# Performance work log

Measured on AMD Instinct MI355X. Metric: run time of the kernel, lower is better.

Reference implementation:

```python
import jax, jax.numpy as jnp
import numpy as np

B, D_IN, HID, DEPTH = 16384, 128, 16, 8
N_INNER = 2 ** DEPTH - 1   # 255
N_LEAF = 2 ** DEPTH        # 256


def setup_inputs() -> dict:
    key = jax.random.key(0)
    ks = jax.random.split(key, 4)
    x = jax.random.normal(ks[0], (B, D_IN), jnp.float32)
    # Batched per-inner-node tiny MLP parameters (PyTorch stores one Sequential per node;
    # we stack them along a leading node axis so the math is identical but vectorized).
    W1 = jax.random.normal(ks[1], (N_INNER, D_IN, HID), jnp.float32) / np.sqrt(D_IN).astype(np.float32)
    b1 = jnp.zeros((N_INNER, HID), jnp.float32)
    W2 = jax.random.normal(ks[2], (N_INNER, HID), jnp.float32) / np.sqrt(HID).astype(np.float32)
    b2 = jnp.zeros((N_INNER,), jnp.float32)
    leaf = jax.random.normal(ks[3], (N_LEAF, 1), jnp.float32) * 0.1
    return {"x": x, "W1": W1, "b1": b1, "W2": W2, "b2": b2, "leaf": leaf}


def reference(x, W1, b1, W2, b2, leaf):
    b = x.shape[0]
    depth = int(np.log2(leaf.shape[0]))
    # All inner-node gates in one batched GEMM: p[b, n] = sigmoid(W2_n . relu(W1_n^T x_b + b1_n) + b2_n)
    h1 = jax.nn.relu(jnp.einsum('bi,nih->bnh', x, W1) + b1[None])  # [B, N_inner, hid]
    p = jax.nn.sigmoid(jnp.einsum('bnh,nh->bn', h1, W2) + b2[None])  # [B, N_inner]

    # Level-by-level probability propagation (heap-ordered nodes):
    # children of node j are 2j+1 (left, mass*(1-p)) and 2j+2 (right, mass*p).
    r = jnp.ones((b, 1), x.dtype)
    levels = []
    for l in range(depth):
        levels.append(r)
        pl = p[:, 2 ** l - 1: 2 ** (l + 1) - 1]  # probs of nodes at level l, [B, 2^l]
        # interleave (left, right) so child ordering matches heap indexing
        r = jnp.stack([r * (1.0 - pl), r * pl], axis=-1).reshape(b, 2 ** (l + 1))
    node_reach = jnp.concatenate(levels, axis=1)  # [B, N_inner]
    path_probs = r                                 # [B, N_leaf]

    h = (path_probs @ leaf)[:, 0]                  # [B]
    return (h, path_probs, p, node_reach)
```

## Files before the change

### kernel.cpp

```cpp
#include <hip/hip_runtime.h>

#define BATCH 16384
#define DIN   128
#define HIDN  16
#define NNODE 255
#define NLEAF 256

typedef _Float16 half8 __attribute__((ext_vector_type(8)));
typedef _Float16 half4 __attribute__((ext_vector_type(4)));
typedef float   float4v __attribute__((ext_vector_type(4)));

__global__ __launch_bounds__(256) void k_pack(const float* __restrict__ x, const float* __restrict__ w1,
                                              const float* __restrict__ w2,
                                              half8* __restrict__ xp, half8* __restrict__ w1p,
                                              _Float16* __restrict__ w2h) {
    __shared__ float w[DIN * 17];
    int t = threadIdx.x;
    if (blockIdx.x < 1024) {
        int gid  = blockIdx.x * 256 + t;
        int lane = gid & 63;
        int kc   = (gid >> 6) & 3;
        int bt   = gid >> 8;
        const float4* src = (const float4*)(x + (size_t)(bt * 16 + (lane & 15)) * DIN + kc * 32 + ((lane >> 4) * 8));
        float4 v0 = src[0], v1 = src[1];
        half8 v;
        v[0] = (_Float16)v0.x; v[1] = (_Float16)v0.y; v[2] = (_Float16)v0.z; v[3] = (_Float16)v0.w;
        v[4] = (_Float16)v1.x; v[5] = (_Float16)v1.y; v[6] = (_Float16)v1.z; v[7] = (_Float16)v1.w;
        xp[gid] = v;
    } else {
        int n = blockIdx.x - 1024;
        const float4* src = (const float4*)(w1 + (size_t)n * (DIN * HIDN)) + t * 2;
        float4 a0 = src[0], a1 = src[1];
        int base = t * 8;
#pragma unroll
        for (int e = 0; e < 4; ++e) {
            int idx0 = base + e, idx1 = base + 4 + e;
            w[(idx0 >> 4) * 17 + (idx0 & 15)] = (&a0.x)[e];
            w[(idx1 >> 4) * 17 + (idx1 & 15)] = (&a1.x)[e];
        }
        __syncthreads();
        int L  = t & 63;
        int kc = t >> 6;
        int m  = L & 15;
        int k0 = kc * 32 + (L >> 4) * 8;
        half8 v;
#pragma unroll
        for (int j = 0; j < 8; ++j) v[j] = (_Float16)w[(k0 + j) * 17 + m];
        w1p[(size_t)n * 256 + t] = v;
        if (t < HIDN) w2h[n * HIDN + t] = (_Float16)w2[n * HIDN + t];
    }
}

__global__ __launch_bounds__(512, 2) void k_fused(const half8* __restrict__ xp, const half8* __restrict__ w1p,
                                                  const float* __restrict__ b1, const _Float16* __restrict__ w2h,
                                                  const float* __restrict__ b2, const float* __restrict__ leaf,
                                                  float* __restrict__ h_out, float* __restrict__ pp_out,
                                                  float* __restrict__ p_out, float* __restrict__ nr_out) {
    __shared__ float sp[64][260];
    int wv   = threadIdx.x >> 6;
    int lane = threadIdx.x & 63;
    int q    = lane >> 4;
    int bt0  = blockIdx.x * 4;

    half8 bq[4][4];
#pragma unroll
    for (int t = 0; t < 4; ++t)
#pragma unroll
        for (int kc = 0; kc < 4; ++kc)
            bq[t][kc] = xp[(size_t)((bt0 + t) * 4 + kc) * 64 + lane];
    asm volatile("" ::: "memory");

    int cnt = (wv < 7) ? 32 : 31;
    int n   = wv;
    half8 a[4];
#pragma unroll
    for (int kc = 0; kc < 4; ++kc) a[kc] = w1p[(size_t)(n * 4 + kc) * 64 + lane];
    float4 b1f = ((const float4*)(b1 + n * HIDN))[q];
    half4  a2  = *(const half4*)(w2h + n * HIDN + q * 4);
    float  b2v = b2[n];

    for (int i = 0; i < cnt; ++i) {
        int nn = n + ((i + 1 < cnt) ? 8 : 0);
        half8 an[4];
#pragma unroll
        for (int kc = 0; kc < 4; ++kc) an[kc] = w1p[(size_t)(nn * 4 + kc) * 64 + lane];
        float4 b1n = ((const float4*)(b1 + nn * HIDN))[q];
        half4  a2n = *(const half4*)(w2h + nn * HIDN + q * 4);
        float  b2n = b2[nn];

#pragma unroll
        for (int t = 0; t < 4; ++t) {
            float4v acc = {b1f.x, b1f.y, b1f.z, b1f.w};
#pragma unroll
            for (int kc = 0; kc < 4; ++kc)
                acc = __builtin_amdgcn_mfma_f32_16x16x32_f16(a[kc], bq[t][kc], acc, 0, 0, 0);
            half4 rb;
#pragma unroll
            for (int r = 0; r < 4; ++r) rb[r] = (_Float16)fmaxf(acc[r], 0.f);
            float4v acc2 = {b2v, b2v, b2v, b2v};
            acc2 = __builtin_amdgcn_mfma_f32_16x16x16f16(a2, rb, acc2, 0, 0, 0);
            if (lane < 16)
                sp[t * 16 + lane][n] =
                    __builtin_amdgcn_rcpf(1.f + __builtin_amdgcn_exp2f(-1.44269504088896f * acc2[0]));
        }
#pragma unroll
        for (int kc = 0; kc < 4; ++kc) a[kc] = an[kc];
        b1f = b1n; a2 = a2n; b2v = b2n;
        n = nn;
    }
    __syncthreads();

    const float4 lf = *(const float4*)(leaf + 4 * lane);
    for (int rr = 0; rr < 8; ++rr) {
        int r = wv * 8 + rr;
        int b = blockIdx.x * 64 + r;
        const float* P = &sp[r][0];
        float* nr = nr_out + (size_t)b * NNODE;

#pragma unroll
        for (int c = 0; c < 4; ++c) {
            int idx = c * 64 + lane;
            if (idx < NNODE)
                p_out[(size_t)b * NNODE + idx] = P[idx];
        }

        float pref = 1.f;
#pragma unroll
        for (int l = 0; l < 6; ++l) {
            if ((lane & ((1 << (6 - l)) - 1)) == 0)
                nr[(1 << l) - 1 + (lane >> (6 - l))] = pref;
            float pv  = P[(1 << l) - 1 + (lane >> (6 - l))];
            int  bit  = (lane >> (5 - l)) & 1;
            pref *= bit ? pv : (1.f - pv);
        }
        nr[63 + lane] = pref;
        float p6 = P[63 + lane];
        float pl = pref * (1.f - p6);
        float pr = pref * p6;
        nr[127 + 2 * lane] = pl;
        nr[128 + 2 * lane] = pr;
        float p7a = P[127 + 2 * lane];
        float p7b = P[128 + 2 * lane];
        float4v pp;
        pp[0] = pl * (1.f - p7a);
        pp[1] = pl * p7a;
        pp[2] = pr * (1.f - p7b);
        pp[3] = pr * p7b;
        *(float4v*)(pp_out + (size_t)b * NLEAF + 4 * lane) = pp;
        float hs = pp[0] * lf.x + pp[1] * lf.y + pp[2] * lf.z + pp[3] * lf.w;
#pragma unroll
        for (int off = 1; off < 64; off <<= 1) hs += __shfl_xor(hs, off, 64);
        if (lane == 0) h_out[b] = hs;
    }
}

extern "C" void kernel_launch(void* const* d_in, const int* in_sizes, int n_in,
                              void* d_out, int out_size, void* d_ws, size_t ws_size,
                              hipStream_t stream) {
    const float* x    = (const float*)d_in[0];
    const float* W1   = (const float*)d_in[1];
    const float* b1   = (const float*)d_in[2];
    const float* W2   = (const float*)d_in[3];
    const float* b2   = (const float*)d_in[4];
    const float* leaf = (const float*)d_in[5];

    float* out    = (float*)d_out;
    float* h_out  = out;
    float* pp_out = out + BATCH;
    float* p_out  = pp_out + (size_t)BATCH * NLEAF;
    float* nr_out = p_out + (size_t)BATCH * NNODE;

    half8*    xp   = (half8*)d_ws;
    half8*    w1p  = xp + (size_t)1024 * 4 * 64;
    _Float16* w2h  = (_Float16*)(w1p + (size_t)NNODE * 256);

    hipLaunchKernelGGL(k_pack,  dim3(1024 + NNODE), dim3(256), 0, stream, x, W1, W2, xp, w1p, w2h);
    hipLaunchKernelGGL(k_fused, dim3(256),          dim3(512), 0, stream,
                       xp, w1p, b1, w2h, b2, leaf, h_out, pp_out, p_out, nr_out);
}
```

Before: 112.1 us.

## Replace second MFMA with FMA dot plus cross-lane shuffle reduction, double-buffer node weights

The second-layer hidden-to-logit projection is now done with per-lane fp32 FMAs and a two-step shuffle reduction instead of a 16x16x16 MFMA on fp16-cast activations, so all 64 lanes write a sigmoid result rather than only 16. The node loop is unrolled by two with separate A/B register buffers, and the next weights are prefetched two nodes ahead. The four batch tiles' MFMAs are interleaved to hide latency, and W2 is read in fp32 directly, which drops its pack step. The cost is more registers and shuffle traffic. Clamping the last node index to 254 makes wave 7 redundantly recompute node 254.

```diff
diff --git a/kernel.cpp b/kernel.cpp
--- a/kernel.cpp
+++ b/kernel.cpp
@@ -7,13 +7,10 @@
 #define NLEAF 256
 
 typedef _Float16 half8 __attribute__((ext_vector_type(8)));
-typedef _Float16 half4 __attribute__((ext_vector_type(4)));
 typedef float   float4v __attribute__((ext_vector_type(4)));
 
 __global__ __launch_bounds__(256) void k_pack(const float* __restrict__ x, const float* __restrict__ w1,
-                                              const float* __restrict__ w2,
-                                              half8* __restrict__ xp, half8* __restrict__ w1p,
-                                              _Float16* __restrict__ w2h) {
+                                              half8* __restrict__ xp, half8* __restrict__ w1p) {
     __shared__ float w[DIN * 17];
     int t = threadIdx.x;
     if (blockIdx.x < 1024) {
@@ -47,12 +44,11 @@
 #pragma unroll
         for (int j = 0; j < 8; ++j) v[j] = (_Float16)w[(k0 + j) * 17 + m];
         w1p[(size_t)n * 256 + t] = v;
-        if (t < HIDN) w2h[n * HIDN + t] = (_Float16)w2[n * HIDN + t];
     }
 }
 
 __global__ __launch_bounds__(512, 2) void k_fused(const half8* __restrict__ xp, const half8* __restrict__ w1p,
-                                                  const float* __restrict__ b1, const _Float16* __restrict__ w2h,
+                                                  const float* __restrict__ b1, const float* __restrict__ w2,
                                                   const float* __restrict__ b2, const float* __restrict__ leaf,
                                                   float* __restrict__ h_out, float* __restrict__ pp_out,
                                                   float* __restrict__ p_out, float* __restrict__ nr_out) {
@@ -70,44 +66,70 @@
             bq[t][kc] = xp[(size_t)((bt0 + t) * 4 + kc) * 64 + lane];
     asm volatile("" ::: "memory");
 
-    int cnt = (wv < 7) ? 32 : 31;
-    int n   = wv;
-    half8 a[4];
-#pragma unroll
-    for (int kc = 0; kc < 4; ++kc) a[kc] = w1p[(size_t)(n * 4 + kc) * 64 + lane];
-    float4 b1f = ((const float4*)(b1 + n * HIDN))[q];
-    half4  a2  = *(const half4*)(w2h + n * HIDN + q * 4);
-    float  b2v = b2[n];
-
-    for (int i = 0; i < cnt; ++i) {
-        int nn = n + ((i + 1 < cnt) ? 8 : 0);
-        half8 an[4];
-#pragma unroll
-        for (int kc = 0; kc < 4; ++kc) an[kc] = w1p[(size_t)(nn * 4 + kc) * 64 + lane];
-        float4 b1n = ((const float4*)(b1 + nn * HIDN))[q];
-        half4  a2n = *(const half4*)(w2h + nn * HIDN + q * 4);
-        float  b2n = b2[nn];
-
-#pragma unroll
-        for (int t = 0; t < 4; ++t) {
-            float4v acc = {b1f.x, b1f.y, b1f.z, b1f.w};
-#pragma unroll
-            for (int kc = 0; kc < 4; ++kc)
-                acc = __builtin_amdgcn_mfma_f32_16x16x32_f16(a[kc], bq[t][kc], acc, 0, 0, 0);
-            half4 rb;
-#pragma unroll
-            for (int r = 0; r < 4; ++r) rb[r] = (_Float16)fmaxf(acc[r], 0.f);
-            float4v acc2 = {b2v, b2v, b2v, b2v};
-            acc2 = __builtin_amdgcn_mfma_f32_16x16x16f16(a2, rb, acc2, 0, 0, 0);
-            if (lane < 16)
-                sp[t * 16 + lane][n] =
-                    __builtin_amdgcn_rcpf(1.f + __builtin_amdgcn_exp2f(-1.44269504088896f * acc2[0]));
-        }
-#pragma unroll
-        for (int kc = 0; kc < 4; ++kc) a[kc] = an[kc];
-        b1f = b1n; a2 = a2n; b2v = b2n;
-        n = nn;
-    }
+    half8  aA[4], aB[4];
+    float4 b1A, b1B, w2A, w2B;
+    float  b2A, b2B;
+
+    int nA = wv;
+#pragma unroll
+    for (int kc = 0; kc < 4; ++kc) aA[kc] = w1p[(size_t)(nA * 4 + kc) * 64 + lane];
+    b1A = ((const float4*)(b1 + nA * HIDN))[q];
+    w2A = ((const float4*)(w2 + nA * HIDN))[q];
+    b2A = b2[nA];
+    {
+        int nB = nA + 8;
+#pragma unroll
+        for (int kc = 0; kc < 4; ++kc) aB[kc] = w1p[(size_t)(nB * 4 + kc) * 64 + lane];
+        b1B = ((const float4*)(b1 + nB * HIDN))[q];
+        w2B = ((const float4*)(w2 + nB * HIDN))[q];
+        b2B = b2[nB];
+    }
+
+#define MLP_BODY(AS, B1S, W2S, B2S, NODE, PREN)                                            \
+    do {                                                                                   \
+        float4v acc0 = {B1S.x, B1S.y, B1S.z, B1S.w};                                       \
+        float4v acc1 = acc0, acc2 = acc0, acc3 = acc0;                                     \
+        _Pragma("unroll") for (int kc = 0; kc < 4; ++kc) {                                 \
+            acc0 = __builtin_amdgcn_mfma_f32_16x16x32_f16(AS[kc], bq[0][kc], acc0, 0, 0, 0);\
+            acc1 = __builtin_amdgcn_mfma_f32_16x16x32_f16(AS[kc], bq[1][kc], acc1, 0, 0, 0);\
+            acc2 = __builtin_amdgcn_mfma_f32_16x16x32_f16(AS[kc], bq[2][kc], acc2, 0, 0, 0);\
+            acc3 = __builtin_amdgcn_mfma_f32_16x16x32_f16(AS[kc], bq[3][kc], acc3, 0, 0, 0);\
+        }                                                                                  \
+        float s0 = fmaf(fmaxf(acc0[0], 0.f), W2S.x, fmaf(fmaxf(acc0[1], 0.f), W2S.y,       \
+                   fmaf(fmaxf(acc0[2], 0.f), W2S.z, fmaxf(acc0[3], 0.f) * W2S.w)));        \
+        float s1 = fmaf(fmaxf(acc1[0], 0.f), W2S.x, fmaf(fmaxf(acc1[1], 0.f), W2S.y,       \
+                   fmaf(fmaxf(acc1[2], 0.f), W2S.z, fmaxf(acc1[3], 0.f) * W2S.w)));        \
+        float s2 = fmaf(fmaxf(acc2[0], 0.f), W2S.x, fmaf(fmaxf(acc2[1], 0.f), W2S.y,       \
+                   fmaf(fmaxf(acc2[2], 0.f), W2S.z, fmaxf(acc2[3], 0.f) * W2S.w)));        \
+        float s3 = fmaf(fmaxf(acc3[0], 0.f), W2S.x, fmaf(fmaxf(acc3[1], 0.f), W2S.y,       \
+                   fmaf(fmaxf(acc3[2], 0.f), W2S.z, fmaxf(acc3[3], 0.f) * W2S.w)));        \
+        float b2c = B2S;                                                                   \
+        _Pragma("unroll") for (int kc = 0; kc < 4; ++kc)                                   \
+            AS[kc] = w1p[(size_t)((PREN) * 4 + kc) * 64 + lane];                           \
+        B1S = ((const float4*)(b1 + (PREN) * HIDN))[q];                                    \
+        W2S = ((const float4*)(w2 + (PREN) * HIDN))[q];                                    \
+        B2S = b2[PREN];                                                                    \
+        int q1 = q & 1, q2 = q & 2;                                                        \
+        float a01 = q1 ? s1 : s0, c01 = q1 ? s0 : s1;                                      \
+        a01 += __shfl_xor(c01, 16, 64);                                                    \
+        float a23 = q1 ? s3 : s2, c23 = q1 ? s2 : s3;                                      \
+        a23 += __shfl_xor(c23, 16, 64);                                                    \
+        float e = q2 ? a23 : a01, f = q2 ? a01 : a23;                                      \
+        e += __shfl_xor(f, 32, 64);                                                        \
+        float lg = e + b2c;                                                                \
+        sp[lane][NODE] =                                                                   \
+            __builtin_amdgcn_rcpf(1.f + __builtin_amdgcn_exp2f(-1.44269504088896f * lg));  \
+    } while (0)
+
+    for (int ii = 0; ii < 16; ++ii) {
+        int pA = nA + 16; pA = pA > 254 ? 254 : pA;
+        MLP_BODY(aA, b1A, w2A, b2A, nA, pA);
+        int nB = nA + 8;  nB = nB > 254 ? 254 : nB;
+        int pB = nA + 24; pB = pB > 254 ? 254 : pB;
+        MLP_BODY(aB, b1B, w2B, b2B, nB, pB);
+        nA += 16;
+    }
+#undef MLP_BODY
     __syncthreads();
 
     const float4 lf = *(const float4*)(leaf + 4 * lane);
@@ -170,11 +192,10 @@
     float* p_out  = pp_out + (size_t)BATCH * NLEAF;
     float* nr_out = p_out + (size_t)BATCH * NNODE;
 
-    half8*    xp   = (half8*)d_ws;
-    half8*    w1p  = xp + (size_t)1024 * 4 * 64;
-    _Float16* w2h  = (_Float16*)(w1p + (size_t)NNODE * 256);
-
-    hipLaunchKernelGGL(k_pack,  dim3(1024 + NNODE), dim3(256), 0, stream, x, W1, W2, xp, w1p, w2h);
+    half8* xp  = (half8*)d_ws;
+    half8* w1p = xp + (size_t)1024 * 4 * 64;
+
+    hipLaunchKernelGGL(k_pack,  dim3(1024 + NNODE), dim3(256), 0, stream, x, W1, xp, w1p);
     hipLaunchKernelGGL(k_fused, dim3(256),          dim3(512), 0, stream,
-                       xp, w1p, b1, w2h, b2, leaf, h_out, pp_out, p_out, nr_out);
+                       xp, w1p, b1, W2, b2, leaf, h_out, pp_out, p_out, nr_out);
 }
```

Measured after the change: 107.2 us. 1.05x faster.
